# Optimization experiments

Measured on AMD Instinct MI355X. Metric: run time of the kernel, lower is better.

## Reference

```python
import jax, jax.numpy as jnp
import numpy as np

LRELU_ALPHA = 0.2       # LeakyReLU slope (alpha arg of GraphAttentionLayer)
NEG_INF = -9e15         # zero_vec value from the torch code
N1, N2, N3 = 3000, 2500, 2500
IN_F, OUT_F, HEADS = 128, 64, 2


def setup_inputs() -> dict:
    key = jax.random.key(0)
    ks = jax.random.split(key, 13)
    N = N1 + N2 + N3
    h = jax.random.normal(ks[0], (N, IN_F), jnp.float32)
    A1  = jax.random.randint(ks[1],  (N1, N1), 0, 2, jnp.int32)
    A2  = jax.random.randint(ks[2],  (N2, N2), 0, 2, jnp.int32)
    A3  = jax.random.randint(ks[3],  (N3, N3), 0, 2, jnp.int32)
    A12 = jax.random.randint(ks[4],  (N1, N2), 0, 2, jnp.int32)
    A13 = jax.random.randint(ks[5],  (N1, N3), 0, 2, jnp.int32)
    A23 = jax.random.randint(ks[6],  (N2, N3), 0, 2, jnp.int32)
    A21 = jax.random.randint(ks[7],  (N2, N1), 0, 2, jnp.int32)
    A31 = jax.random.randint(ks[8],  (N3, N1), 0, 2, jnp.int32)
    A32 = jax.random.randint(ks[9],  (N3, N2), 0, 2, jnp.int32)
    # per-head GAT parameters (xavier-ish scale)
    Ws = jax.random.normal(ks[10], (HEADS, IN_F, OUT_F), jnp.float32) * 0.12
    a_param = jax.random.normal(ks[11], (HEADS, 2 * OUT_F, 1), jnp.float32) * 0.12
    return dict(h=h, A1=A1, A2=A2, A3=A3, A12=A12, A13=A13, A23=A23,
                A21=A21, A31=A31, A32=A32, Ws=Ws, a_param=a_param)


def reference(h, A1, A2, A3, A12, A13, A23, A21, A31, A32, Ws, a_param):
    n1, n2, n3 = A1.shape[0], A2.shape[0], A3.shape[0]
    # The 9 block assignments in the torch forward tile the full NxN matrix,
    # so they are equivalent to one block-structured mask.
    mask = jnp.block([[A1,  A12, A13],
                      [A21, A2,  A23],
                      [A31, A32, A3]]) > 0          # [N, N] bool

    Wh = jnp.einsum('nf,hfo->hno', h, Ws)           # [H, N, O]
    a1 = a_param[:, :OUT_F, 0]                      # [H, O]
    a2 = a_param[:, OUT_F:, 0]                      # [H, O]
    Wh1 = jnp.einsum('hno,ho->hn', Wh, a1)          # [H, N]
    Wh2 = jnp.einsum('hno,ho->hn', Wh, a2)          # [H, N]
    e = jax.nn.leaky_relu(Wh1[:, :, None] + Wh2[:, None, :], LRELU_ALPHA)  # [H,N,N]
    att = jax.nn.softmax(jnp.where(mask[None], e, NEG_INF), axis=-1)
    # dropout is identity in eval mode
    mid = jnp.einsum('hij,hjo->hio', att, Wh)       # [H, N, O]
    out = jax.nn.elu(mid)                           # concat=True -> elu
    x2 = out.transpose(1, 0, 2).reshape(h.shape[0], -1)  # [N, H*O] head concat

    x3 = jax.nn.log_softmax(x2[n1 + n2:], axis=1)   # group-3 nodes
    x4 = jax.nn.log_softmax(x2[:n1], axis=1)        # group-1 nodes
    x5 = jax.nn.log_softmax(x2[n1:n1 + n2], axis=1) # group-2 nodes
    return (x3, x4, x5)
```

## Files before the change

kernel.cpp:

```cpp
#include <hip/hip_runtime.h>
#include <hip/hip_bf16.h>


#define CN1 3000
#define CN2 2500
#define CN3 2500
#define NTOT 8000
#define INF_ 128
#define OUTF 64
#define LOG2E 1.44269504088896340736f
#define ALPHA 0.2f

typedef __attribute__((ext_vector_type(4))) float f32x4;
typedef __attribute__((ext_vector_type(8))) short short8;
typedef __attribute__((ext_vector_type(4))) int i32x4;
union B16x8 { int4 i4; short8 s8; unsigned int u[4]; };

#if defined(__has_builtin)
#if __has_builtin(__builtin_amdgcn_exp2f)
#define EXP2F(x) __builtin_amdgcn_exp2f(x)
#endif
#endif
#ifndef EXP2F
#define EXP2F(x) exp2f(x)
#endif

__device__ inline float wave_sum(float v) {
  for (int d = 32; d; d >>= 1) v += __shfl_xor(v, d, 64);
  return v;
}

__device__ inline unsigned int pk2(float a, float b) {
  union { __hip_bfloat162 h; unsigned int u; } cv;
  cv.h = __float22bfloat162_rn(make_float2(a, b));
  return cv.u;
}

__device__ inline unsigned int pack2_bf16(float a, float b) {
  unsigned ua = __float_as_uint(a);
  ua = (ua + 0x7FFFu + ((ua >> 16) & 1u)) >> 16;
  unsigned ub = __float_as_uint(b);
  ub = (ub + 0x7FFFu + ((ub >> 16) & 1u)) & 0xFFFF0000u;
  return ub | ua;
}

__global__ __launch_bounds__(256)
void k_front(const int* __restrict__ A1,  const int* __restrict__ A12, const int* __restrict__ A13,
             const int* __restrict__ A21, const int* __restrict__ A2,  const int* __restrict__ A23,
             const int* __restrict__ A31, const int* __restrict__ A32, const int* __restrict__ A3,
             unsigned int* __restrict__ packed,
             const float* __restrict__ hv, const float* __restrict__ Wsv,
             const float* __restrict__ ap,
             float* __restrict__ Whf,
             float* __restrict__ Wh1s,
             float* __restrict__ Wh2s,
             unsigned int* __restrict__ E2pk) {
  if ((blockIdx.x & 1) == 0) {
    const int i = (blockIdx.x >> 1) * 4 + (threadIdx.x >> 6);
    const int lane = threadIdx.x & 63;
    const int *r0, *r1, *r2;
    if (i < CN1)            { r0 = A1  + i * CN1;          r1 = A12 + i * CN2;          r2 = A13 + i * CN3; }
    else if (i < CN1 + CN2) { int r = i - CN1;       r0 = A21 + r * CN1; r1 = A2  + r * CN2; r2 = A23 + r * CN3; }
    else                    { int r = i - CN1 - CN2; r0 = A31 + r * CN1; r1 = A32 + r * CN2; r2 = A3  + r * CN3; }
    const i32x4* p0 = (const i32x4*)r0;
    const i32x4* p1 = (const i32x4*)r1;
    const i32x4* p2 = (const i32x4*)r2;
    unsigned int* pkrow = packed + (i >> 4) * 4000 + (i & 15);
    const int sh = 4 * (lane & 7);
    const int w  = lane >> 3;
#pragma unroll
    for (int ob = 0; ob < 2; ++ob) {
      i32x4 v[16];
#pragma unroll
      for (int u = 0; u < 16; ++u) {
        int q = (ob * 16 + u) * 64 + lane;
        q = q < 2000 ? q : 1999;
        const i32x4* src = (q < 750) ? (p0 + q) : (q < 1375) ? (p1 + q - 750) : (p2 + q - 1375);
        v[u] = __builtin_nontemporal_load(src);
      }
#pragma unroll
      for (int u = 0; u < 16; ++u) {
        const int it = ob * 16 + u;
        const bool act = (it * 64 + lane) < 2000;
        unsigned int n = (v[u].x > 0 ? 1u : 0u) | (v[u].y > 0 ? 2u : 0u)
                       | (v[u].z > 0 ? 4u : 0u) | (v[u].w > 0 ? 8u : 0u);
        n = act ? (n << sh) : 0u;
        n |= __shfl_xor(n, 1, 64);
        n |= __shfl_xor(n, 2, 64);
        n |= __shfl_xor(n, 4, 64);
        const int wglob = it * 8 + w;
        if ((lane & 7) == 0 && wglob < 250)
          pkrow[wglob * 16] = n;
      }
    }
  } else {
    const int t = threadIdx.x;
    const int o = t & 63;
    const int n = (blockIdx.x >> 1) * 4 + (t >> 6);
    const float* hrow = hv + n * INF_;
    const float* Ws0 = Wsv + o;
    const float* Ws1 = Wsv + INF_ * OUTF + o;
    float a0a = 0.f, a0b = 0.f, a1a = 0.f, a1b = 0.f;
#pragma unroll 8
    for (int f = 0; f < INF_; f += 2) {
      float h0 = hrow[f], h1 = hrow[f + 1];
      a0a += h0 * Ws0[f * OUTF];
      a0b += h1 * Ws0[(f + 1) * OUTF];
      a1a += h0 * Ws1[f * OUTF];
      a1b += h1 * Ws1[(f + 1) * OUTF];
    }
    float acc0 = a0a + a0b, acc1 = a1a + a1b;
    Whf[(0 * NTOT + n) * OUTF + o] = acc0;
    Whf[(1 * NTOT + n) * OUTF + o] = acc1;
    float s10 = wave_sum(acc0 * ap[o]);
    float s20 = wave_sum(acc0 * ap[OUTF + o]);
    float s11 = wave_sum(acc1 * ap[2 * OUTF + o]);
    float s21 = wave_sum(acc1 * ap[3 * OUTF + o]);
    if (o == 0) {
      const float w20 = s20 * LOG2E, w21 = s21 * LOG2E;
      Wh1s[n] = s10 * LOG2E;        Wh2s[n] = w20;
      Wh1s[NTOT + n] = s11 * LOG2E; Wh2s[NTOT + n] = w21;
      E2pk[n]        = pk2(EXP2F(w20), EXP2F(ALPHA * w20));
      E2pk[NTOT + n] = pk2(EXP2F(w21), EXP2F(ALPHA * w21));
    }
  }
}

__global__ __launch_bounds__(256)
void k_mid(const float* __restrict__ Whf, const float* __restrict__ Wh2s,
           float* __restrict__ M2s, int4* __restrict__ WhB) {
  if (blockIdx.x < 2) {
    const int hd = blockIdx.x;
    float mx = -1e30f;
    for (int i = threadIdx.x; i < NTOT; i += 256)
      mx = fmaxf(mx, Wh2s[hd * NTOT + i]);
    for (int d = 32; d; d >>= 1) mx = fmaxf(mx, __shfl_xor(mx, d, 64));
    __shared__ float red[4];
    if ((threadIdx.x & 63) == 0) red[threadIdx.x >> 6] = mx;
    __syncthreads();
    if (threadIdx.x == 0)
      M2s[hd] = fmaxf(fmaxf(red[0], red[1]), fmaxf(red[2], red[3]));
  } else {
    const int gid = (blockIdx.x - 2) * 256 + threadIdx.x;
    const int lane = gid & 63;
    const int c = (gid >> 6) & 3;
    const int t = (gid >> 8) % 250;
    const int hd = gid / 64000;
    const int jb = t * 32 + (lane >> 4) * 8;
    const int col = c * 16 + (lane & 15);
    const float* src = Whf + (hd * NTOT + jb) * OUTF + col;
    B16x8 out;
#pragma unroll
    for (int e2 = 0; e2 < 4; ++e2)
      out.u[e2] = pack2_bf16(src[(2 * e2) * OUTF], src[(2 * e2 + 1) * OUTF]);
    WhB[gid] = out.i4;
  }
}

__global__ __launch_bounds__(128)
void k_attn_mfma(const unsigned int* __restrict__ packed,
                 const float* __restrict__ Wh1s,
                 const float* __restrict__ M2s, const int4* __restrict__ WhB,
                 const unsigned int* __restrict__ E2pk,
                 float* __restrict__ partAcc,
                 float* __restrict__ partS)
{
  const int hd = threadIdx.x >> 6;
  const int lane = threadIdx.x & 63;
  const int m = lane & 15;
  const int g = lane >> 4;
  const int kb = g * 8;
  const int rbA = blockIdx.x * 2;
  const int rbB = rbA + 1;
  const int iA = rbA * 16 + m;
  const int iB = rbB * 16 + m;
  const int jy = blockIdx.y, njy = gridDim.y;
  const int t0 = (250 * jy) / njy, t1 = (250 * (jy + 1)) / njy;

  const unsigned int* pkbA = packed + rbA * 4000 + m;
  const unsigned int* pkbB = packed + rbB * 4000 + m;

  const float w1sA = Wh1s[hd * NTOT + iA];
  const float w1sB = Wh1s[hd * NTOT + iB];
  const float yA = w1sA + M2s[hd], yB = w1sB + M2s[hd];
  const float ciA = fmaxf(yA, ALPHA * yA), ciB = fmaxf(yB, ALPHA * yB);
  const float E1pA = EXP2F(w1sA - ciA), E1nA = EXP2F(fmaf(ALPHA, w1sA, -ciA));
  const float E1pB = EXP2F(w1sB - ciB), E1nB = EXP2F(fmaf(ALPHA, w1sB, -ciB));
  const unsigned int* e2 = E2pk + hd * NTOT;
  const int4* WhBh = WhB + hd * 64000;

  f32x4 aA_0 = {0.f,0.f,0.f,0.f}, aA_1 = aA_0, aA_2 = aA_0, aA_3 = aA_0;
  f32x4 aB_0 = aA_0, aB_1 = aA_0, aB_2 = aA_0, aB_3 = aA_0;
  f32x4 svA = aA_0, svB = aA_0;

  B16x8 ones;
#pragma unroll
  for (int e2i = 0; e2i < 4; ++e2i) ones.u[e2i] = 0x3F803F80u;

  struct Frags { int4 f[4]; uint4 ua, ub; };
  auto load_frags = [&](int t, Frags& F) {
    const int4* bp = WhBh + t * 256 + lane;
#pragma unroll
    for (int c = 0; c < 4; ++c) F.f[c] = bp[c * 64];
    const unsigned int* w0 = e2 + t * 32 + kb;
    F.ua = *(const uint4*)w0; F.ub = *(const uint4*)(w0 + 4);
  };

  auto compute = [&](unsigned int mwA, unsigned int mwB, const Frags& F) {
    const unsigned bitsA = (mwA >> kb) & 0xffu;
    const unsigned bitsB = (mwB >> kb) & 0xffu;
    const unsigned uv[8] = {F.ua.x, F.ua.y, F.ua.z, F.ua.w, F.ub.x, F.ub.y, F.ub.z, F.ub.w};
    float qA[8], qB[8];
#pragma unroll
    for (int e = 0; e < 8; ++e) {
      float p = __uint_as_float(uv[e] << 16);
      float nn = __uint_as_float(uv[e] & 0xFFFF0000u);
      float vA = fmaxf(E1pA * p, E1nA * nn);
      float vB = fmaxf(E1pB * p, E1nB * nn);
      qA[e] = ((bitsA >> e) & 1u) ? vA : 0.f;
      qB[e] = ((bitsB >> e) & 1u) ? vB : 0.f;
    }
    B16x8 afA, afB;
#pragma unroll
    for (int e2i = 0; e2i < 4; ++e2i) {
      afA.u[e2i] = pk2(qA[2 * e2i], qA[2 * e2i + 1]);
      afB.u[e2i] = pk2(qB[2 * e2i], qB[2 * e2i + 1]);
    }
    B16x8 b;
    b.i4 = F.f[0];
    aA_0 = __builtin_amdgcn_mfma_f32_16x16x32_bf16(afA.s8, b.s8, aA_0, 0, 0, 0);
    aB_0 = __builtin_amdgcn_mfma_f32_16x16x32_bf16(afB.s8, b.s8, aB_0, 0, 0, 0);
    b.i4 = F.f[1];
    aA_1 = __builtin_amdgcn_mfma_f32_16x16x32_bf16(afA.s8, b.s8, aA_1, 0, 0, 0);
    aB_1 = __builtin_amdgcn_mfma_f32_16x16x32_bf16(afB.s8, b.s8, aB_1, 0, 0, 0);
    b.i4 = F.f[2];
    aA_2 = __builtin_amdgcn_mfma_f32_16x16x32_bf16(afA.s8, b.s8, aA_2, 0, 0, 0);
    aB_2 = __builtin_amdgcn_mfma_f32_16x16x32_bf16(afB.s8, b.s8, aB_2, 0, 0, 0);
    b.i4 = F.f[3];
    aA_3 = __builtin_amdgcn_mfma_f32_16x16x32_bf16(afA.s8, b.s8, aA_3, 0, 0, 0);
    aB_3 = __builtin_amdgcn_mfma_f32_16x16x32_bf16(afB.s8, b.s8, aB_3, 0, 0, 0);
    svA = __builtin_amdgcn_mfma_f32_16x16x32_bf16(afA.s8, ones.s8, svA, 0, 0, 0);
    svB = __builtin_amdgcn_mfma_f32_16x16x32_bf16(afB.s8, ones.s8, svB, 0, 0, 0);
  };

  unsigned int mwA0 = pkbA[t0 * 16],                 mwB0 = pkbB[t0 * 16];
  unsigned int mwA1 = pkbA[min(t0 + 1, t1 - 1) * 16], mwB1 = pkbB[min(t0 + 1, t1 - 1) * 16];
  Frags FA, FB;
  load_frags(t0, FA);
  int t = t0;
  for (; t + 1 < t1; t += 2) {
    load_frags(t + 1, FB);
    const int tna = min(t + 2, t1 - 1);
    unsigned int mwAa = pkbA[tna * 16], mwBa = pkbB[tna * 16];
    compute(mwA0, mwB0, FA);
    mwA0 = mwA1; mwB0 = mwB1; mwA1 = mwAa; mwB1 = mwBa;
    load_frags(tna, FA);
    const int tnb = min(t + 3, t1 - 1);
    unsigned int mwAb = pkbA[tnb * 16], mwBb = pkbB[tnb * 16];
    compute(mwA0, mwB0, FB);
    mwA0 = mwA1; mwB0 = mwB1; mwA1 = mwAb; mwB1 = mwBb;
  }
  if (t < t1) compute(mwA0, mwB0, FA);

  const int baseA = (jy * 2 + hd) * NTOT + rbA * 16;
  const int baseB = (jy * 2 + hd) * NTOT + rbB * 16;
  if (m == 0) {
#pragma unroll
    for (int q = 0; q < 4; ++q) {
      partS[baseA + g * 4 + q] = svA[q];
      partS[baseB + g * 4 + q] = svB[q];
    }
  }
  float* oA = partAcc + baseA * OUTF;
  float* oB = partAcc + baseB * OUTF;
#pragma unroll
  for (int q = 0; q < 4; ++q) {
    const int row = g * 4 + q;
    oA[row * OUTF +      m] = aA_0[q];
    oA[row * OUTF + 16 + m] = aA_1[q];
    oA[row * OUTF + 32 + m] = aA_2[q];
    oA[row * OUTF + 48 + m] = aA_3[q];
    oB[row * OUTF +      m] = aB_0[q];
    oB[row * OUTF + 16 + m] = aB_1[q];
    oB[row * OUTF + 32 + m] = aB_2[q];
    oB[row * OUTF + 48 + m] = aB_3[q];
  }
}

__global__ void k_final(const float* __restrict__ partAcc, const float* __restrict__ partS,
                        int njy, float* __restrict__ out) {
  const int wave = threadIdx.x >> 6, lane = threadIdx.x & 63;
  const int n = blockIdx.x * 4 + wave;
  float x[2];
#pragma unroll
  for (int hd = 0; hd < 2; ++hd) {
    float a = 0.f, s = 0.f;
    for (int jy = 0; jy < njy; ++jy) {
      a += partAcc[((jy * 2 + hd) * NTOT + n) * OUTF + lane];
      s += partS[(jy * 2 + hd) * NTOT + n];
    }
    float mid = a / s;
    x[hd] = mid > 0.f ? mid : (__expf(mid) - 1.f);
  }
  float mx = fmaxf(x[0], x[1]);
  for (int d = 32; d; d >>= 1) mx = fmaxf(mx, __shfl_xor(mx, d, 64));
  float se = __expf(x[0] - mx) + __expf(x[1] - mx);
  for (int d = 32; d; d >>= 1) se += __shfl_xor(se, d, 64);
  const float lse = mx + __logf(se);
  const int orow = (n >= CN1 + CN2) ? (n - CN1 - CN2) : (n + CN3);
  out[orow * 128 + lane]      = x[0] - lse;
  out[orow * 128 + 64 + lane] = x[1] - lse;
}

__global__ void k_sentinel(float* __restrict__ out, float v) {
  out[blockIdx.x * 256 + threadIdx.x] = v;
}

extern "C" void kernel_launch(void* const* d_in, const int* in_sizes, int n_in,
                              void* d_out, int out_size, void* d_ws, size_t ws_size,
                              hipStream_t stream) {
  float* outf = (float*)d_out;

  static const int EXP[12] = {1024000, 9000000, 6250000, 6250000, 7500000, 7500000,
                              6250000, 7500000, 7500000, 6250000, 16384, 256};
  bool exact = (n_in == 12);
  if (exact) for (int i = 0; i < 12; ++i) if (in_sizes[i] != EXP[i]) { exact = false; break; }

  const size_t FIXED = 64000 + 64000 + 256 + 64000 + 2048000 + 8000000;
  int njy = 0;
  for (int cand = 8; cand >= 1; cand >>= 1) {
    size_t need = FIXED + (size_t)cand * 64000 + (size_t)cand * 4096000;
    if (ws_size >= need) { njy = cand; break; }
  }
  if (!exact || njy == 0) {
    k_sentinel<<<dim3(4000), dim3(256), 0, stream>>>(outf, -148.0f);
    return;
  }

  const float* h  = (const float*)d_in[0];
  const int* A1  = (const int*)d_in[1];
  const int* A2  = (const int*)d_in[2];
  const int* A3  = (const int*)d_in[3];
  const int* A12 = (const int*)d_in[4];
  const int* A13 = (const int*)d_in[5];
  const int* A23 = (const int*)d_in[6];
  const int* A21 = (const int*)d_in[7];
  const int* A31 = (const int*)d_in[8];
  const int* A32 = (const int*)d_in[9];
  const float* Ws = (const float*)d_in[10];
  const float* ap = (const float*)d_in[11];

  char* w = (char*)d_ws;
  float*        Wh1s    = (float*)(w);
  float*        Wh2s    = (float*)(w + 64000);
  float*        M2s     = (float*)(w + 128000);
  unsigned int* E2pk    = (unsigned int*)(w + 128256);
  int4*         WhB     = (int4*) (w + 192256);
  unsigned int* packed  = (unsigned int*)(w + 2240256);
  float*        partS   = (float*)(w + 10240256);
  float*        Whf     = (float*)(w + 10240256 + (size_t)njy * 64000);
  float*        partAcc = Whf;

  k_front    <<<dim3(4000),     dim3(256), 0, stream>>>(A1, A12, A13, A21, A2, A23, A31, A32, A3,
                                                        packed, h, Ws, ap, Whf, Wh1s, Wh2s, E2pk);
  k_mid      <<<dim3(502),      dim3(256), 0, stream>>>(Whf, Wh2s, M2s, WhB);
  k_attn_mfma<<<dim3(250, njy), dim3(128), 0, stream>>>(packed, Wh1s, M2s, WhB, E2pk,
                                                        partAcc, partS);
  k_final    <<<dim3(2000),     dim3(256), 0, stream>>>(partAcc, partS, njy, outf);
}
```

Baseline: 329.5 us.

## Fuse bf16 Wh fragment packing into front kernel and drop fp32 Wh buffer

The projection half of k_front now computes eight nodes per wave for one head, packs the results to bf16 and writes them directly in the MFMA fragment layout. This removes the fp32 Wh intermediate and most of the k_mid kernel, leaving a tiny max-reduction kernel. The block role split changes from 1:1 to 4:1 mask-packing versus projection blocks, so mask packing gets more of the grid. The cost is more per-thread register accumulators in the projection path and strided loads of h rows.

```diff
diff --git a/kernel.cpp b/kernel.cpp
--- a/kernel.cpp
+++ b/kernel.cpp
@@ -36,14 +36,6 @@
   return cv.u;
 }
 
-__device__ inline unsigned int pack2_bf16(float a, float b) {
-  unsigned ua = __float_as_uint(a);
-  ua = (ua + 0x7FFFu + ((ua >> 16) & 1u)) >> 16;
-  unsigned ub = __float_as_uint(b);
-  ub = (ub + 0x7FFFu + ((ub >> 16) & 1u)) & 0xFFFF0000u;
-  return ub | ua;
-}
-
 __global__ __launch_bounds__(256)
 void k_front(const int* __restrict__ A1,  const int* __restrict__ A12, const int* __restrict__ A13,
              const int* __restrict__ A21, const int* __restrict__ A2,  const int* __restrict__ A23,
@@ -51,12 +43,13 @@
              unsigned int* __restrict__ packed,
              const float* __restrict__ hv, const float* __restrict__ Wsv,
              const float* __restrict__ ap,
-             float* __restrict__ Whf,
              float* __restrict__ Wh1s,
              float* __restrict__ Wh2s,
-             unsigned int* __restrict__ E2pk) {
-  if ((blockIdx.x & 1) == 0) {
-    const int i = (blockIdx.x >> 1) * 4 + (threadIdx.x >> 6);
+             unsigned int* __restrict__ E2pk,
+             int4* __restrict__ WhB) {
+  const int role = blockIdx.x % 5;
+  if (role < 4) {
+    const int i = ((blockIdx.x / 5) * 4 + role) * 4 + (threadIdx.x >> 6);
     const int lane = threadIdx.x & 63;
     const int *r0, *r1, *r2;
     if (i < CN1)            { r0 = A1  + i * CN1;          r1 = A12 + i * CN2;          r2 = A13 + i * CN3; }
@@ -94,67 +87,55 @@
       }
     }
   } else {
-    const int t = threadIdx.x;
-    const int o = t & 63;
-    const int n = (blockIdx.x >> 1) * 4 + (t >> 6);
-    const float* hrow = hv + n * INF_;
-    const float* Ws0 = Wsv + o;
-    const float* Ws1 = Wsv + INF_ * OUTF + o;
-    float a0a = 0.f, a0b = 0.f, a1a = 0.f, a1b = 0.f;
-#pragma unroll 8
-    for (int f = 0; f < INF_; f += 2) {
-      float h0 = hrow[f], h1 = hrow[f + 1];
-      a0a += h0 * Ws0[f * OUTF];
-      a0b += h1 * Ws0[(f + 1) * OUTF];
-      a1a += h0 * Ws1[f * OUTF];
-      a1b += h1 * Ws1[(f + 1) * OUTF];
-    }
-    float acc0 = a0a + a0b, acc1 = a1a + a1b;
-    Whf[(0 * NTOT + n) * OUTF + o] = acc0;
-    Whf[(1 * NTOT + n) * OUTF + o] = acc1;
-    float s10 = wave_sum(acc0 * ap[o]);
-    float s20 = wave_sum(acc0 * ap[OUTF + o]);
-    float s11 = wave_sum(acc1 * ap[2 * OUTF + o]);
-    float s21 = wave_sum(acc1 * ap[3 * OUTF + o]);
-    if (o == 0) {
-      const float w20 = s20 * LOG2E, w21 = s21 * LOG2E;
-      Wh1s[n] = s10 * LOG2E;        Wh2s[n] = w20;
-      Wh1s[NTOT + n] = s11 * LOG2E; Wh2s[NTOT + n] = w21;
-      E2pk[n]        = pk2(EXP2F(w20), EXP2F(ALPHA * w20));
-      E2pk[NTOT + n] = pk2(EXP2F(w21), EXP2F(ALPHA * w21));
+    const int u = blockIdx.x / 5;
+    const int hd = u & 1;
+    const int tg = u >> 1;
+    const int wv = threadIdx.x >> 6;
+    const int lane = threadIdx.x & 63;
+    const int n0 = tg * 32 + wv * 8;
+    const float* Wsh = Wsv + hd * (INF_ * OUTF) + lane;
+    const float* h0 = hv + n0 * INF_;
+    float acc[8] = {0.f,0.f,0.f,0.f,0.f,0.f,0.f,0.f};
+#pragma unroll 4
+    for (int f = 0; f < INF_; ++f) {
+      const float wsv = Wsh[f * OUTF];
+#pragma unroll
+      for (int k = 0; k < 8; ++k)
+        acc[k] = fmaf(h0[k * INF_ + f], wsv, acc[k]);
+    }
+    B16x8 fr;
+#pragma unroll
+    for (int e = 0; e < 4; ++e) fr.u[e] = pk2(acc[2 * e], acc[2 * e + 1]);
+    WhB[hd * 64000 + tg * 256 + (lane >> 4) * 64 + wv * 16 + (lane & 15)] = fr.i4;
+    const float a1v = ap[hd * 128 + lane];
+    const float a2v = ap[hd * 128 + 64 + lane];
+#pragma unroll
+    for (int k = 0; k < 8; ++k) {
+      float s1 = wave_sum(acc[k] * a1v);
+      float s2 = wave_sum(acc[k] * a2v);
+      if (lane == 0) {
+        const int n = n0 + k;
+        const float w2 = s2 * LOG2E;
+        Wh1s[hd * NTOT + n] = s1 * LOG2E;
+        Wh2s[hd * NTOT + n] = w2;
+        E2pk[hd * NTOT + n] = pk2(EXP2F(w2), EXP2F(ALPHA * w2));
+      }
     }
   }
 }
 
 __global__ __launch_bounds__(256)
-void k_mid(const float* __restrict__ Whf, const float* __restrict__ Wh2s,
-           float* __restrict__ M2s, int4* __restrict__ WhB) {
-  if (blockIdx.x < 2) {
-    const int hd = blockIdx.x;
-    float mx = -1e30f;
-    for (int i = threadIdx.x; i < NTOT; i += 256)
-      mx = fmaxf(mx, Wh2s[hd * NTOT + i]);
-    for (int d = 32; d; d >>= 1) mx = fmaxf(mx, __shfl_xor(mx, d, 64));
-    __shared__ float red[4];
-    if ((threadIdx.x & 63) == 0) red[threadIdx.x >> 6] = mx;
-    __syncthreads();
-    if (threadIdx.x == 0)
-      M2s[hd] = fmaxf(fmaxf(red[0], red[1]), fmaxf(red[2], red[3]));
-  } else {
-    const int gid = (blockIdx.x - 2) * 256 + threadIdx.x;
-    const int lane = gid & 63;
-    const int c = (gid >> 6) & 3;
-    const int t = (gid >> 8) % 250;
-    const int hd = gid / 64000;
-    const int jb = t * 32 + (lane >> 4) * 8;
-    const int col = c * 16 + (lane & 15);
-    const float* src = Whf + (hd * NTOT + jb) * OUTF + col;
-    B16x8 out;
-#pragma unroll
-    for (int e2 = 0; e2 < 4; ++e2)
-      out.u[e2] = pack2_bf16(src[(2 * e2) * OUTF], src[(2 * e2 + 1) * OUTF]);
-    WhB[gid] = out.i4;
-  }
+void k_m2(const float* __restrict__ Wh2s, float* __restrict__ M2s) {
+  const int hd = blockIdx.x;
+  float mx = -1e30f;
+  for (int i = threadIdx.x; i < NTOT; i += 256)
+    mx = fmaxf(mx, Wh2s[hd * NTOT + i]);
+  for (int d = 32; d; d >>= 1) mx = fmaxf(mx, __shfl_xor(mx, d, 64));
+  __shared__ float red[4];
+  if ((threadIdx.x & 63) == 0) red[threadIdx.x >> 6] = mx;
+  __syncthreads();
+  if (threadIdx.x == 0)
+    M2s[hd] = fmaxf(fmaxf(red[0], red[1]), fmaxf(red[2], red[3]));
 }
 
 __global__ __launch_bounds__(128)
@@ -358,12 +339,11 @@
   int4*         WhB     = (int4*) (w + 192256);
   unsigned int* packed  = (unsigned int*)(w + 2240256);
   float*        partS   = (float*)(w + 10240256);
-  float*        Whf     = (float*)(w + 10240256 + (size_t)njy * 64000);
-  float*        partAcc = Whf;
-
-  k_front    <<<dim3(4000),     dim3(256), 0, stream>>>(A1, A12, A13, A21, A2, A23, A31, A32, A3,
-                                                        packed, h, Ws, ap, Whf, Wh1s, Wh2s, E2pk);
-  k_mid      <<<dim3(502),      dim3(256), 0, stream>>>(Whf, Wh2s, M2s, WhB);
+  float*        partAcc = (float*)(w + 10240256 + (size_t)njy * 64000);
+
+  k_front    <<<dim3(2500),     dim3(256), 0, stream>>>(A1, A12, A13, A21, A2, A23, A31, A32, A3,
+                                                        packed, h, Ws, ap, Wh1s, Wh2s, E2pk, WhB);
+  k_m2       <<<dim3(2),        dim3(256), 0, stream>>>(Wh2s, M2s);
   k_attn_mfma<<<dim3(250, njy), dim3(128), 0, stream>>>(packed, Wh1s, M2s, WhB, E2pk,
                                                         partAcc, partS);
   k_final    <<<dim3(2000),     dim3(256), 0, stream>>>(partAcc, partS, njy, outf);
```

Measured after the change: 329.0 us. Within noise of the previous version (-0.1%).
